# Kernel optimization log

Measured on AMD Instinct MI355X. Metric: run time of the kernel, lower is better.

The kernel has to match this reference:

```python
import jax, jax.numpy as jnp
import numpy as np

IN_C, C_M, C_N, K = 512, 512, 128, 1
B, H, W = 8, 64, 64

def setup_inputs() -> dict:
    key = jax.random.key(0)
    ks = jax.random.split(key, 8)
    s = 1.0 / np.sqrt(IN_C)
    return {
        "x": jax.random.normal(ks[0], (B, IN_C, H, W), dtype=jnp.float32),
        "y": jax.random.normal(ks[1], (B, C_M, H, W), dtype=jnp.float32),
        "wA": jax.random.uniform(ks[2], (C_M, IN_C), minval=-s, maxval=s, dtype=jnp.float32),
        "bA": jax.random.uniform(ks[3], (C_M,), minval=-s, maxval=s, dtype=jnp.float32),
        "wB": jax.random.uniform(ks[4], (C_N, IN_C), minval=-s, maxval=s, dtype=jnp.float32),
        "bB": jax.random.uniform(ks[5], (C_N,), minval=-s, maxval=s, dtype=jnp.float32),
        "wV": jax.random.uniform(ks[6], (C_N, IN_C), minval=-s, maxval=s, dtype=jnp.float32),
        "bV": jax.random.uniform(ks[7], (C_N,), minval=-s, maxval=s, dtype=jnp.float32),
    }

def reference(x, y, wA, bA, wB, bB, wV, bV):
    # A2-Net double attention, K=1 so batch = b1 and K*h*w = N.
    b, c, h, w = x.shape
    N = h * w
    xf = x.reshape(b, c, N)                                  # [b, C, N]
    A = jnp.einsum('mc,bcn->bmn', wA, xf) + bA[:, None]      # [b, c_m, N]
    Bf = jnp.einsum('kc,bcn->bkn', wB, xf) + bB[:, None]     # [b, c_n, N]
    V = jnp.einsum('kc,bcn->bkn', wV, xf) + bV[:, None]      # [b, c_n, N]
    # tmpB viewed (b*c_n, N), softmax dim=1 -> softmax over N per (b, c_n) row
    softB = jax.nn.softmax(Bf, axis=-1)                      # [b, c_n, N]
    # tmpV viewed (b*N, c_n), softmax dim=1 -> softmax over c_n per pixel
    softV = jax.nn.softmax(V, axis=1)                        # [b, c_n, N]
    # gather: tmpG = tmpA @ softB^T  -> [b, c_m, c_n]
    G = jnp.einsum('bmn,bkn->bmk', A, softB)
    # distribute: tmpZ = G @ softV -> [b, c_m, N]
    Z = jnp.einsum('bmk,bkn->bmn', G, softV)
    return Z.reshape(b, -1, h, w) + y
```

## Files before the change

### kernel.cpp

```cpp
#include <hip/hip_runtime.h>

#define BATCH 8
#define INC 512
#define CM 512
#define CN 128
#define NPIX 4096
#define NSPLIT 8

typedef short bf16x8 __attribute__((ext_vector_type(8)));
typedef float f32x4 __attribute__((ext_vector_type(4)));
typedef unsigned short us8v __attribute__((ext_vector_type(8)));

__device__ __forceinline__ unsigned short f2b(float f) {
    union { float f; unsigned u; } v; v.f = f;
    unsigned r = v.u + 0x7FFF + ((v.u >> 16) & 1);
    return (unsigned short)(r >> 16);
}
__device__ __forceinline__ float b2f(unsigned short u) {
    union { unsigned u; float f; } v; v.u = ((unsigned)u) << 16;
    return v.f;
}

__device__ __forceinline__ void gl_lds16(const unsigned short* g, unsigned short* l) {
    __builtin_amdgcn_global_load_lds(
        (const __attribute__((address_space(1))) unsigned int*)g,
        (__attribute__((address_space(3))) unsigned int*)l, 16, 0, 0);
}

__device__ __forceinline__ void stage_tile(const unsigned short* src, int ld, int kbase,
                                           unsigned short* lds, int t) {
    #pragma unroll
    for (int q = 0; q < 2; ++q) {
        int f = q * 256 + t;
        const unsigned short* g = src + (size_t)(f >> 2) * ld + kbase + (f & 3) * 8;
        gl_lds16(g, lds + f * 8);
    }
}

__device__ __forceinline__ void bt_compute(const unsigned short* lA, const unsigned short* lB,
                                           f32x4 acc[4][4], int wr, int wc, int lane) {
    int lr = lane & 15, lq = lane >> 4;
    bf16x8 av[4], bv[4];
    #pragma unroll
    for (int i = 0; i < 4; ++i)
        av[i] = *(const bf16x8*)&lA[(wr * 64 + i * 16 + lr) * 32 + lq * 8];
    #pragma unroll
    for (int j = 0; j < 4; ++j)
        bv[j] = *(const bf16x8*)&lB[(wc * 64 + j * 16 + lr) * 32 + lq * 8];
    #pragma unroll
    for (int i = 0; i < 4; ++i)
        #pragma unroll
        for (int j = 0; j < 4; ++j)
            acc[i][j] = __builtin_amdgcn_mfma_f32_16x16x32_bf16(av[i], bv[j], acc[i][j], 0, 0, 0);
}

#define ZERO_ACC(acc)                       \
    f32x4 acc[4][4];                        \
    {                                       \
        f32x4 z4 = {0.f, 0.f, 0.f, 0.f};   \
        for (int i = 0; i < 4; ++i)         \
            for (int j = 0; j < 4; ++j)     \
                acc[i][j] = z4;             \
    }

__device__ __forceinline__ void ep_stage(float* ep, const f32x4 (*acc)[4],
                                         int ch, int wr, int wc, int lane) {
    if (wr == (ch >> 1)) {
        int lr = lane & 15, lq = lane >> 4;
        int ibase = (ch & 1) * 2;
        #pragma unroll
        for (int ii = 0; ii < 2; ++ii) {
            #pragma unroll
            for (int j = 0; j < 4; ++j)
                #pragma unroll
                for (int reg = 0; reg < 4; ++reg)
                    ep[(ii * 16 + lq * 4 + reg) * 132 + wc * 64 + j * 16 + lr] =
                        acc[ibase + ii][j][reg];
        }
    }
}

__global__ __launch_bounds__(256) void k_prep(
    const float* __restrict__ x, const float* __restrict__ wA,
    const float* __restrict__ wB, const float* __restrict__ wV,
    unsigned short* __restrict__ xT, unsigned short* __restrict__ x16,
    unsigned short* __restrict__ wA16, unsigned short* __restrict__ wB16,
    unsigned short* __restrict__ wV16)
{
    if (blockIdx.z == BATCH) {
        int bl = blockIdx.y * 64 + blockIdx.x;
        if (bl >= 384) return;
        int e = (bl * 256 + threadIdx.x) * 4;
        const float* src; unsigned short* dst; int off;
        if (e < 262144)       { src = wA; dst = wA16; off = e; }
        else if (e < 327680)  { src = wB; dst = wB16; off = e - 262144; }
        else                  { src = wV; dst = wV16; off = e - 327680; }
        float4 v = *(const float4*)&src[off];
        *(ushort4*)&dst[off] = make_ushort4(f2b(v.x), f2b(v.y), f2b(v.z), f2b(v.w));
        return;
    }
    __shared__ unsigned short tile[64][68];
    int n0 = blockIdx.x * 64, c0 = blockIdx.y * 64, b = blockIdx.z;
    int t = threadIdx.x;
    int tr = t >> 4, tc4 = (t & 15) * 4;
    const float* xb = x + ((size_t)b * INC + c0) * NPIX + n0;
    unsigned short* x16p = x16 + ((size_t)b * INC + c0) * NPIX + n0;
    #pragma unroll
    for (int p = 0; p < 4; ++p) {
        int r = p * 16 + tr;
        float4 v = *(const float4*)&xb[(size_t)r * NPIX + tc4];
        ushort4 u = make_ushort4(f2b(v.x), f2b(v.y), f2b(v.z), f2b(v.w));
        *(ushort4*)&x16p[(size_t)r * NPIX + tc4] = u;
        tile[r][tc4 + 0] = u.x; tile[r][tc4 + 1] = u.y;
        tile[r][tc4 + 2] = u.z; tile[r][tc4 + 3] = u.w;
    }
    __syncthreads();
    unsigned short* o = xT + ((size_t)b * NPIX + n0) * INC + c0;
    #pragma unroll
    for (int p = 0; p < 4; ++p) {
        int n = p * 16 + tr;
        ushort4 u = make_ushort4(tile[tc4 + 0][n], tile[tc4 + 1][n],
                                 tile[tc4 + 2][n], tile[tc4 + 3][n]);
        *(ushort4*)&o[(size_t)n * INC + tc4] = u;
    }
}

__global__ __launch_bounds__(256) void k_proj(
    const unsigned short* __restrict__ xT, const unsigned short* __restrict__ wB16,
    const unsigned short* __restrict__ wV16, const float* __restrict__ bB,
    const float* __restrict__ bV, unsigned short* __restrict__ Bf16,
    unsigned short* __restrict__ V16)
{
    __shared__ __align__(16) char smem[32 * 132 * 4];
    unsigned short* lA = (unsigned short*)smem;
    unsigned short* lB = lA + 4096;
    int t = threadIdx.x;
    int n0 = blockIdx.x * 128;
    int z = blockIdx.y, b = z >> 1, br = z & 1;
    const unsigned short* A = br ? wV16 : wB16;
    const float* bias = br ? bV : bB;
    unsigned short* out = br ? V16 : Bf16;
    const unsigned short* Bm = xT + ((size_t)b * NPIX + n0) * INC;

    ZERO_ACC(acc);
    int lane = t & 63, w = t >> 6, wr = w >> 1, wc = w & 1;

    for (int c = 0; c < INC; c += 32) {
        stage_tile(A, INC, c, lA, t);
        stage_tile(Bm, INC, c, lB, t);
        __syncthreads();
        bt_compute(lA, lB, acc, wr, wc, lane);
        __syncthreads();
    }
    float* ep = (float*)smem;
    #pragma unroll
    for (int ch = 0; ch < 4; ++ch) {
        __syncthreads();
        ep_stage(ep, acc, ch, wr, wc, lane);
        __syncthreads();
        int r = t >> 3, c4 = (t & 7) * 16;
        int k = ch * 32 + r;
        float bv_ = bias[k];
        unsigned short* op = out + ((size_t)b * CN + k) * NPIX + n0 + c4;
        #pragma unroll
        for (int h = 0; h < 2; ++h) {
            us8v o;
            #pragma unroll
            for (int j = 0; j < 8; ++j) o[j] = f2b(ep[r * 132 + c4 + h * 8 + j] + bv_);
            *(us8v*)&op[h * 8] = o;
        }
    }
}

__global__ __launch_bounds__(256) void k_softmax_rows(
    const unsigned short* __restrict__ Bf16, unsigned short* __restrict__ sB)
{
    __shared__ float red[8];
    int row = blockIdx.x, t = threadIdx.x;
    const unsigned short* p = Bf16 + (size_t)row * NPIX + t * 16;
    us8v u0 = *(const us8v*)p, u1 = *(const us8v*)(p + 8);
    float v[16];
    #pragma unroll
    for (int j = 0; j < 8; ++j) { v[j] = b2f(u0[j]); v[8 + j] = b2f(u1[j]); }
    float m = -1e30f;
    #pragma unroll
    for (int j = 0; j < 16; ++j) m = fmaxf(m, v[j]);
    for (int o = 32; o > 0; o >>= 1) m = fmaxf(m, __shfl_xor(m, o));
    if ((t & 63) == 0) red[t >> 6] = m;
    __syncthreads();
    m = fmaxf(fmaxf(red[0], red[1]), fmaxf(red[2], red[3]));
    float s = 0.f;
    #pragma unroll
    for (int j = 0; j < 16; ++j) { v[j] = __expf(v[j] - m); s += v[j]; }
    for (int o = 32; o > 0; o >>= 1) s += __shfl_xor(s, o);
    if ((t & 63) == 0) red[4 + (t >> 6)] = s;
    __syncthreads();
    float r = 1.0f / (red[4] + red[5] + red[6] + red[7]);
    us8v o0, o1;
    #pragma unroll
    for (int j = 0; j < 8; ++j) { o0[j] = f2b(v[j] * r); o1[j] = f2b(v[8 + j] * r); }
    unsigned short* q = sB + (size_t)row * NPIX + t * 16;
    *(us8v*)q = o0; *(us8v*)(q + 8) = o1;
}

__global__ __launch_bounds__(256) void k_softmax_cols(
    const unsigned short* __restrict__ V16, unsigned short* __restrict__ sVt)
{
    __shared__ unsigned short tv[128][138];
    __shared__ float pm[2][128], ps[2][128], sm[128], sr[128];
    int n0 = blockIdx.x * 128, b = blockIdx.y, t = threadIdx.x;
    const unsigned short* vb = V16 + (size_t)b * CN * NPIX + n0;
    #pragma unroll
    for (int it = 0; it < 8; ++it) {
        int f = it * 256 + t, k = f >> 4, n8 = (f & 15) * 8;
        us8v u = *(const us8v*)&vb[(size_t)k * NPIX + n8];
        #pragma unroll
        for (int j = 0; j < 8; ++j) tv[n8 + j][k] = u[j];
    }
    __syncthreads();
    {
        int p = t & 127, h = t >> 7;
        float m = -1e30f;
        for (int k = h * 64; k < h * 64 + 64; ++k) m = fmaxf(m, b2f(tv[p][k]));
        float s = 0.f;
        for (int k = h * 64; k < h * 64 + 64; ++k) s += __expf(b2f(tv[p][k]) - m);
        pm[h][p] = m; ps[h][p] = s;
    }
    __syncthreads();
    if (t < 128) {
        float ma = pm[0][t], mb = pm[1][t];
        float m = fmaxf(ma, mb);
        float s = ps[0][t] * __expf(ma - m) + ps[1][t] * __expf(mb - m);
        sm[t] = m; sr[t] = 1.0f / s;
    }
    __syncthreads();
    unsigned short* ob = sVt + ((size_t)b * NPIX + n0) * CN;
    #pragma unroll
    for (int it = 0; it < 8; ++it) {
        int idx = it * 2048 + t * 8, nl = idx >> 7, k0 = idx & 127;
        float m = sm[nl], r = sr[nl];
        us8v o;
        #pragma unroll
        for (int j = 0; j < 8; ++j) o[j] = f2b(__expf(b2f(tv[nl][k0 + j]) - m) * r);
        *(us8v*)&ob[(size_t)nl * CN + k0] = o;
    }
}

__global__ __launch_bounds__(256) void k_gather(
    const unsigned short* __restrict__ x16, const unsigned short* __restrict__ sB,
    float* __restrict__ Pts)
{
    __shared__ __align__(16) char smem[32 * 132 * 4];
    unsigned short* lA = (unsigned short*)smem;
    unsigned short* lB = lA + 4096;
    int t = threadIdx.x;
    int c0 = blockIdx.x * 128, s = blockIdx.y, b = blockIdx.z;
    const unsigned short* A = sB + (size_t)b * CN * NPIX;
    const unsigned short* Bm = x16 + ((size_t)b * INC + c0) * NPIX;
    int nbase = s * (NPIX / NSPLIT);

    ZERO_ACC(acc);
    int lane = t & 63, w = t >> 6, wr = w >> 1, wc = w & 1;

    for (int it = 0; it < (NPIX / NSPLIT) / 32; ++it) {
        int nb = nbase + it * 32;
        stage_tile(A, NPIX, nb, lA, t);
        stage_tile(Bm, NPIX, nb, lB, t);
        __syncthreads();
        bt_compute(lA, lB, acc, wr, wc, lane);
        __syncthreads();
    }
    float* ep = (float*)smem;
    #pragma unroll
    for (int ch = 0; ch < 4; ++ch) {
        __syncthreads();
        ep_stage(ep, acc, ch, wr, wc, lane);
        __syncthreads();
        int r = t >> 3, c4 = (t & 7) * 16;
        int k = ch * 32 + r;
        float* op = &Pts[(((size_t)s * BATCH + b) * CN + k) * INC + c0 + c4];
        #pragma unroll
        for (int q = 0; q < 4; ++q)
            *(float4*)&op[q * 4] = *(float4*)&ep[r * 132 + c4 + q * 4];
    }
}

__global__ __launch_bounds__(256) void k_reduceP(
    const float* __restrict__ Pts, unsigned short* __restrict__ Pt16)
{
    int base = (blockIdx.x * 256 + threadIdx.x) * 4;
    float4 sacc = make_float4(0.f, 0.f, 0.f, 0.f);
    #pragma unroll
    for (int sp = 0; sp < NSPLIT; ++sp) {
        float4 v = *(const float4*)&Pts[(size_t)sp * (BATCH * CN * INC) + base];
        sacc.x += v.x; sacc.y += v.y; sacc.z += v.z; sacc.w += v.w;
    }
    *(ushort4*)&Pt16[base] = make_ushort4(f2b(sacc.x), f2b(sacc.y), f2b(sacc.z), f2b(sacc.w));
}

__global__ __launch_bounds__(256) void k_G(
    const unsigned short* __restrict__ wA16, const float* __restrict__ bA,
    const unsigned short* __restrict__ Pt16, unsigned short* __restrict__ G16)
{
    __shared__ __align__(16) char smem[32 * 132 * 4];
    unsigned short* lA = (unsigned short*)smem;
    unsigned short* lB = lA + 4096;
    int t = threadIdx.x;
    int m0 = blockIdx.x * 128, b = blockIdx.y;
    const unsigned short* A = wA16 + (size_t)m0 * INC;
    const unsigned short* Bm = Pt16 + (size_t)b * CN * INC;

    ZERO_ACC(acc);
    int lane = t & 63, w = t >> 6, wr = w >> 1, wc = w & 1;

    for (int c = 0; c < INC; c += 32) {
        stage_tile(A, INC, c, lA, t);
        stage_tile(Bm, INC, c, lB, t);
        __syncthreads();
        bt_compute(lA, lB, acc, wr, wc, lane);
        __syncthreads();
    }
    float* ep = (float*)smem;
    #pragma unroll
    for (int ch = 0; ch < 4; ++ch) {
        __syncthreads();
        ep_stage(ep, acc, ch, wr, wc, lane);
        __syncthreads();
        int r = t >> 3, c4 = (t & 7) * 16;
        int m = m0 + ch * 32 + r;
        float bv_ = bA[m];
        unsigned short* op = G16 + ((size_t)b * CM + m) * CN + c4;
        #pragma unroll
        for (int h = 0; h < 2; ++h) {
            us8v o;
            #pragma unroll
            for (int j = 0; j < 8; ++j) o[j] = f2b(ep[r * 132 + c4 + h * 8 + j] + bv_);
            *(us8v*)&op[h * 8] = o;
        }
    }
}

__global__ __launch_bounds__(256) void k_Z(
    const unsigned short* __restrict__ G16, const unsigned short* __restrict__ sVt,
    const float* __restrict__ y, float* __restrict__ out)
{
    __shared__ __align__(16) char smem[32 * 132 * 4];
    unsigned short* lA = (unsigned short*)smem;
    unsigned short* lB = lA + 4096;
    int t = threadIdx.x;
    int n0 = blockIdx.x * 128, m0 = blockIdx.y * 128, b = blockIdx.z;
    const unsigned short* A = G16 + ((size_t)b * CM + m0) * CN;
    const unsigned short* Bm = sVt + ((size_t)b * NPIX + n0) * CN;

    ZERO_ACC(acc);
    int lane = t & 63, w = t >> 6, wr = w >> 1, wc = w & 1;

    for (int kc = 0; kc < CN; kc += 32) {
        stage_tile(A, CN, kc, lA, t);
        stage_tile(Bm, CN, kc, lB, t);
        __syncthreads();
        bt_compute(lA, lB, acc, wr, wc, lane);
        __syncthreads();
    }
    float* ep = (float*)smem;
    #pragma unroll
    for (int ch = 0; ch < 4; ++ch) {
        __syncthreads();
        ep_stage(ep, acc, ch, wr, wc, lane);
        __syncthreads();
        int r = t >> 3, c4 = (t & 7) * 16;
        int m = m0 + ch * 32 + r;
        size_t base = ((size_t)b * CM + m) * NPIX + n0 + c4;
        #pragma unroll
        for (int q = 0; q < 4; ++q) {
            float4 a = *(float4*)&ep[r * 132 + c4 + q * 4];
            float4 yv = *(const float4*)&y[base + q * 4];
            a.x += yv.x; a.y += yv.y; a.z += yv.z; a.w += yv.w;
            *(float4*)&out[base + q * 4] = a;
        }
    }
}

extern "C" void kernel_launch(void* const* d_in, const int* in_sizes, int n_in,
                              void* d_out, int out_size, void* d_ws, size_t ws_size,
                              hipStream_t stream)
{
    const float* x  = (const float*)d_in[0];
    const float* y  = (const float*)d_in[1];
    const float* wA = (const float*)d_in[2];
    const float* bA = (const float*)d_in[3];
    const float* wB = (const float*)d_in[4];
    const float* bB = (const float*)d_in[5];
    const float* wV = (const float*)d_in[6];
    const float* bV = (const float*)d_in[7];
    float* out = (float*)d_out;

    unsigned short* xT16 = (unsigned short*)d_ws;
    unsigned short* x16  = xT16 + 16777216;
    unsigned short* wA16 = x16  + 16777216;
    unsigned short* wB16 = wA16 + 262144;
    unsigned short* wV16 = wB16 + 65536;
    unsigned short* Bf16 = wV16 + 65536;
    unsigned short* V16  = Bf16 + 4194304;
    unsigned short* sB   = V16  + 4194304;
    unsigned short* sVt  = sB   + 4194304;
    unsigned short* Pt16 = sVt  + 4194304;
    float*  Pts = (float*)(Pt16 + 524288);
    unsigned short* G16  = (unsigned short*)(Pts + (size_t)NSPLIT * BATCH * CN * INC);

    k_prep<<<dim3(64, 8, BATCH + 1), 256, 0, stream>>>(
        x, wA, wB, wV, xT16, x16, wA16, wB16, wV16);
    k_proj<<<dim3(NPIX / 128, BATCH * 2), 256, 0, stream>>>(
        xT16, wB16, wV16, bB, bV, Bf16, V16);
    k_softmax_rows<<<dim3(BATCH * CN), 256, 0, stream>>>(Bf16, sB);
    k_softmax_cols<<<dim3(NPIX / 128, BATCH), 256, 0, stream>>>(V16, sVt);
    k_gather<<<dim3(INC / 128, NSPLIT, BATCH), 256, 0, stream>>>(x16, sB, Pts);
    k_reduceP<<<512, 256, 0, stream>>>(Pts, Pt16);
    k_G<<<dim3(CM / 128, BATCH), 256, 0, stream>>>(wA16, bA, Pt16, G16);
    k_Z<<<dim3(NPIX / 128, CM / 128, BATCH), 256, 0, stream>>>(G16, sVt, y, out);
}
```

Before: 266.4 us.

## Double-buffer LDS tiles in GEMM kernels and write epilogue directly from registers

Replaces the single-buffered stage/sync/compute/sync loop in four GEMM kernels with a shared double-buffered pipeline, so the next K-tile loads into LDS while the current one is computed, with one barrier per iteration. The LDS-staged epilogue is dropped; each lane writes its MFMA accumulators straight to global memory with bias or residual applied. This removes the epilogue barriers and LDS round trips, but the stores become scalar 16-lane-strided writes instead of vectorised 16-byte writes, and LDS usage grows to 32 KB per block.

```diff
diff --git a/kernel.cpp b/kernel.cpp
--- a/kernel.cpp
+++ b/kernel.cpp
@@ -63,21 +63,25 @@
                 acc[i][j] = z4;             \
     }
 
-__device__ __forceinline__ void ep_stage(float* ep, const f32x4 (*acc)[4],
-                                         int ch, int wr, int wc, int lane) {
-    if (wr == (ch >> 1)) {
-        int lr = lane & 15, lq = lane >> 4;
-        int ibase = (ch & 1) * 2;
-        #pragma unroll
-        for (int ii = 0; ii < 2; ++ii) {
-            #pragma unroll
-            for (int j = 0; j < 4; ++j)
-                #pragma unroll
-                for (int reg = 0; reg < 4; ++reg)
-                    ep[(ii * 16 + lq * 4 + reg) * 132 + wc * 64 + j * 16 + lr] =
-                        acc[ibase + ii][j][reg];
-        }
-    }
+__device__ __forceinline__ void pipe_loop(const unsigned short* A, int lda,
+                                          const unsigned short* Bm, int ldb,
+                                          int kbase, int nt,
+                                          unsigned short* lds, f32x4 acc[4][4],
+                                          int t, int wr, int wc, int lane)
+{
+    stage_tile(A, lda, kbase, lds, t);
+    stage_tile(Bm, ldb, kbase, lds + 4096, t);
+    __syncthreads();
+    int cur = 0;
+    for (int it = 0; it < nt - 1; ++it) {
+        unsigned short* nb = lds + ((cur ^ 1) << 13);
+        stage_tile(A, lda, kbase + (it + 1) * 32, nb, t);
+        stage_tile(Bm, ldb, kbase + (it + 1) * 32, nb + 4096, t);
+        bt_compute(lds + (cur << 13), lds + (cur << 13) + 4096, acc, wr, wc, lane);
+        __syncthreads();
+        cur ^= 1;
+    }
+    bt_compute(lds + (cur << 13), lds + (cur << 13) + 4096, acc, wr, wc, lane);
 }
 
 __global__ __launch_bounds__(256) void k_prep(
@@ -131,9 +135,7 @@
     const float* __restrict__ bV, unsigned short* __restrict__ Bf16,
     unsigned short* __restrict__ V16)
 {
-    __shared__ __align__(16) char smem[32 * 132 * 4];
-    unsigned short* lA = (unsigned short*)smem;
-    unsigned short* lB = lA + 4096;
+    __shared__ __align__(16) unsigned short lds[16384];
     int t = threadIdx.x;
     int n0 = blockIdx.x * 128;
     int z = blockIdx.y, b = z >> 1, br = z & 1;
@@ -145,31 +147,21 @@
     ZERO_ACC(acc);
     int lane = t & 63, w = t >> 6, wr = w >> 1, wc = w & 1;
 
-    for (int c = 0; c < INC; c += 32) {
-        stage_tile(A, INC, c, lA, t);
-        stage_tile(Bm, INC, c, lB, t);
-        __syncthreads();
-        bt_compute(lA, lB, acc, wr, wc, lane);
-        __syncthreads();
-    }
-    float* ep = (float*)smem;
-    #pragma unroll
-    for (int ch = 0; ch < 4; ++ch) {
-        __syncthreads();
-        ep_stage(ep, acc, ch, wr, wc, lane);
-        __syncthreads();
-        int r = t >> 3, c4 = (t & 7) * 16;
-        int k = ch * 32 + r;
-        float bv_ = bias[k];
-        unsigned short* op = out + ((size_t)b * CN + k) * NPIX + n0 + c4;
-        #pragma unroll
-        for (int h = 0; h < 2; ++h) {
-            us8v o;
+    pipe_loop(A, INC, Bm, INC, 0, INC / 32, lds, acc, t, wr, wc, lane);
+
+    int lr = lane & 15, lq = lane >> 4;
+    int r0 = wr * 64 + lq * 4;
+    unsigned short* op = out + (size_t)b * CN * NPIX + n0 + wc * 64 + lr;
+    #pragma unroll
+    for (int i = 0; i < 4; ++i)
+        #pragma unroll
+        for (int reg = 0; reg < 4; ++reg) {
+            int k = r0 + i * 16 + reg;
+            float bv_ = bias[k];
             #pragma unroll
-            for (int j = 0; j < 8; ++j) o[j] = f2b(ep[r * 132 + c4 + h * 8 + j] + bv_);
-            *(us8v*)&op[h * 8] = o;
+            for (int j = 0; j < 4; ++j)
+                op[(size_t)k * NPIX + j * 16] = f2b(acc[i][j][reg] + bv_);
         }
-    }
 }
 
 __global__ __launch_bounds__(256) void k_softmax_rows(
@@ -250,9 +242,7 @@
     const unsigned short* __restrict__ x16, const unsigned short* __restrict__ sB,
     float* __restrict__ Pts)
 {
-    __shared__ __align__(16) char smem[32 * 132 * 4];
-    unsigned short* lA = (unsigned short*)smem;
-    unsigned short* lB = lA + 4096;
+    __shared__ __align__(16) unsigned short lds[16384];
     int t = threadIdx.x;
     int c0 = blockIdx.x * 128, s = blockIdx.y, b = blockIdx.z;
     const unsigned short* A = sB + (size_t)b * CN * NPIX;
@@ -262,27 +252,20 @@
     ZERO_ACC(acc);
     int lane = t & 63, w = t >> 6, wr = w >> 1, wc = w & 1;
 
-    for (int it = 0; it < (NPIX / NSPLIT) / 32; ++it) {
-        int nb = nbase + it * 32;
-        stage_tile(A, NPIX, nb, lA, t);
-        stage_tile(Bm, NPIX, nb, lB, t);
-        __syncthreads();
-        bt_compute(lA, lB, acc, wr, wc, lane);
-        __syncthreads();
-    }
-    float* ep = (float*)smem;
-    #pragma unroll
-    for (int ch = 0; ch < 4; ++ch) {
-        __syncthreads();
-        ep_stage(ep, acc, ch, wr, wc, lane);
-        __syncthreads();
-        int r = t >> 3, c4 = (t & 7) * 16;
-        int k = ch * 32 + r;
-        float* op = &Pts[(((size_t)s * BATCH + b) * CN + k) * INC + c0 + c4];
-        #pragma unroll
-        for (int q = 0; q < 4; ++q)
-            *(float4*)&op[q * 4] = *(float4*)&ep[r * 132 + c4 + q * 4];
-    }
+    pipe_loop(A, NPIX, Bm, NPIX, nbase, (NPIX / NSPLIT) / 32, lds, acc, t, wr, wc, lane);
+
+    int lr = lane & 15, lq = lane >> 4;
+    int r0 = wr * 64 + lq * 4;
+    float* op = Pts + ((size_t)s * BATCH + b) * CN * INC + c0 + wc * 64 + lr;
+    #pragma unroll
+    for (int i = 0; i < 4; ++i)
+        #pragma unroll
+        for (int reg = 0; reg < 4; ++reg) {
+            int k = r0 + i * 16 + reg;
+            #pragma unroll
+            for (int j = 0; j < 4; ++j)
+                op[(size_t)k * INC + j * 16] = acc[i][j][reg];
+        }
 }
 
 __global__ __launch_bounds__(256) void k_reduceP(
@@ -302,9 +285,7 @@
     const unsigned short* __restrict__ wA16, const float* __restrict__ bA,
     const unsigned short* __restrict__ Pt16, unsigned short* __restrict__ G16)
 {
-    __shared__ __align__(16) char smem[32 * 132 * 4];
-    unsigned short* lA = (unsigned short*)smem;
-    unsigned short* lB = lA + 4096;
+    __shared__ __align__(16) unsigned short lds[16384];
     int t = threadIdx.x;
     int m0 = blockIdx.x * 128, b = blockIdx.y;
     const unsigned short* A = wA16 + (size_t)m0 * INC;
@@ -313,40 +294,28 @@
     ZERO_ACC(acc);
     int lane = t & 63, w = t >> 6, wr = w >> 1, wc = w & 1;
 
-    for (int c = 0; c < INC; c += 32) {
-        stage_tile(A, INC, c, lA, t);
-        stage_tile(Bm, INC, c, lB, t);
-        __syncthreads();
-        bt_compute(lA, lB, acc, wr, wc, lane);
-        __syncthreads();
-    }
-    float* ep = (float*)smem;
-    #pragma unroll
-    for (int ch = 0; ch < 4; ++ch) {
-        __syncthreads();
-        ep_stage(ep, acc, ch, wr, wc, lane);
-        __syncthreads();
-        int r = t >> 3, c4 = (t & 7) * 16;
-        int m = m0 + ch * 32 + r;
-        float bv_ = bA[m];
-        unsigned short* op = G16 + ((size_t)b * CM + m) * CN + c4;
-        #pragma unroll
-        for (int h = 0; h < 2; ++h) {
-            us8v o;
+    pipe_loop(A, INC, Bm, INC, 0, INC / 32, lds, acc, t, wr, wc, lane);
+
+    int lr = lane & 15, lq = lane >> 4;
+    int r0 = wr * 64 + lq * 4;
+    unsigned short* op = G16 + ((size_t)b * CM + m0) * CN + wc * 64 + lr;
+    #pragma unroll
+    for (int i = 0; i < 4; ++i)
+        #pragma unroll
+        for (int reg = 0; reg < 4; ++reg) {
+            int mloc = r0 + i * 16 + reg;
+            float bv_ = bA[m0 + mloc];
             #pragma unroll
-            for (int j = 0; j < 8; ++j) o[j] = f2b(ep[r * 132 + c4 + h * 8 + j] + bv_);
-            *(us8v*)&op[h * 8] = o;
+            for (int j = 0; j < 4; ++j)
+                op[(size_t)mloc * CN + j * 16] = f2b(acc[i][j][reg] + bv_);
         }
-    }
 }
 
 __global__ __launch_bounds__(256) void k_Z(
     const unsigned short* __restrict__ G16, const unsigned short* __restrict__ sVt,
     const float* __restrict__ y, float* __restrict__ out)
 {
-    __shared__ __align__(16) char smem[32 * 132 * 4];
-    unsigned short* lA = (unsigned short*)smem;
-    unsigned short* lB = lA + 4096;
+    __shared__ __align__(16) unsigned short lds[16384];
     int t = threadIdx.x;
     int n0 = blockIdx.x * 128, m0 = blockIdx.y * 128, b = blockIdx.z;
     const unsigned short* A = G16 + ((size_t)b * CM + m0) * CN;
@@ -355,30 +324,19 @@
     ZERO_ACC(acc);
     int lane = t & 63, w = t >> 6, wr = w >> 1, wc = w & 1;
 
-    for (int kc = 0; kc < CN; kc += 32) {
-        stage_tile(A, CN, kc, lA, t);
-        stage_tile(Bm, CN, kc, lB, t);
-        __syncthreads();
-        bt_compute(lA, lB, acc, wr, wc, lane);
-        __syncthreads();
-    }
-    float* ep = (float*)smem;
-    #pragma unroll
-    for (int ch = 0; ch < 4; ++ch) {
-        __syncthreads();
-        ep_stage(ep, acc, ch, wr, wc, lane);
-        __syncthreads();
-        int r = t >> 3, c4 = (t & 7) * 16;
-        int m = m0 + ch * 32 + r;
-        size_t base = ((size_t)b * CM + m) * NPIX + n0 + c4;
-        #pragma unroll
-        for (int q = 0; q < 4; ++q) {
-            float4 a = *(float4*)&ep[r * 132 + c4 + q * 4];
-            float4 yv = *(const float4*)&y[base + q * 4];
-            a.x += yv.x; a.y += yv.y; a.z += yv.z; a.w += yv.w;
-            *(float4*)&out[base + q * 4] = a;
+    pipe_loop(A, CN, Bm, CN, 0, CN / 32, lds, acc, t, wr, wc, lane);
+
+    int lr = lane & 15, lq = lane >> 4;
+    size_t rbase = ((size_t)b * CM + m0 + wr * 64 + lq * 4) * NPIX + n0 + wc * 64 + lr;
+    #pragma unroll
+    for (int i = 0; i < 4; ++i)
+        #pragma unroll
+        for (int reg = 0; reg < 4; ++reg) {
+            size_t ro = rbase + (size_t)(i * 16 + reg) * NPIX;
+            #pragma unroll
+            for (int j = 0; j < 4; ++j)
+                out[ro + j * 16] = acc[i][j][reg] + y[ro + j * 16];
         }
-    }
 }
 
 extern "C" void kernel_launch(void* const* d_in, const int* in_sizes, int n_in,
```

Result: faster. 253.3 us (-4.9%).
